# Kernel tuning notes

Hardware: AMD Instinct MI355X
Metric: run time of the kernel (lower is better)

Reference implementation:

```python
import jax, jax.numpy as jnp
import numpy as np

B, S, CIN, WIDTH, COUT = 8, 256, 3, 64, 1
MODES, BW = 32, 3


def _dct_matrix(n):
    # orthonormal DCT-II matrix; inverse = transpose (DCT-III)
    k = np.arange(n)[:, None].astype(np.float64)
    x = np.arange(n)[None, :].astype(np.float64)
    m = np.sqrt(2.0 / n) * np.cos(np.pi * (x + 0.5) * k / n)
    m[0] *= 1.0 / np.sqrt(2.0)
    return jnp.asarray(m, dtype=jnp.float32)

DCT = _dct_matrix(S)  # [S, S]


def T_fwd(u):  # u: [B, C, H, W] -> spectral coefficients
    u = jnp.einsum('kh,bchw->bckw', DCT, u)
    return jnp.einsum('lw,bckw->bckl', DCT, u)


def T_inv(c):  # inverse transform (orthonormal => transpose)
    c = jnp.einsum('kh,bckw->bchw', DCT, c)
    return jnp.einsum('lw,bclw->bclh', DCT, c).transpose(0, 1, 3, 2)


def T_inv2(c):
    # straightforward version: apply M^T along both spatial dims
    c = jnp.einsum('kh,bckl->bchl', DCT, c)
    return jnp.einsum('lw,bchl->bchw', DCT, c)


def gelu(x):
    return jax.nn.gelu(x, approximate=False)


def pseudo_spectra(u, w, cout):
    # u: [B, Cin, S, S]; w: [Cin*BW*BW, cout, MODES*MODES]
    b = T_fwd(u)
    p = MODES + BW - 1
    bp = b[:, :, :p, :p]  # pad_slices (triL=0)
    # im2col matching torch.nn.Unfold channel-major ordering (c, ki, kj)
    patches = jnp.stack([bp[:, :, i:i + MODES, j:j + MODES]
                         for i in range(BW) for j in range(BW)], axis=2)
    bs, cin = u.shape[0], u.shape[1]
    xp = patches.reshape(bs, cin * BW * BW, MODES * MODES)
    om = jnp.einsum('bix,iox->box', xp, w).reshape(bs, cout, MODES, MODES)
    out = jnp.zeros((bs, cout, S, S), u.dtype).at[:, :, :MODES, :MODES].set(om)
    return T_inv2(out)


def conv1x1(x, w, b):
    return jnp.einsum('oi,bihw->bohw', w, x) + b[None, :, None, None]


def setup_inputs() -> dict:
    key = jax.random.key(0)
    ks = jax.random.split(key, 20)
    mm = MODES * MODES
    inp = {'x': jax.random.normal(ks[0], (B, S, S, CIN), dtype=jnp.float32)}
    # PseudoSpectra weights: scale * U[0,1), scale = 1/(in*out)
    inp['wl'] = jax.random.uniform(ks[1], (CIN * BW * BW, WIDTH - CIN, mm), dtype=jnp.float32) / (CIN * (WIDTH - CIN))
    for i in range(4):
        inp[f'wc{i}'] = jax.random.uniform(ks[2 + i], (WIDTH * BW * BW, WIDTH, mm), dtype=jnp.float32) / (WIDTH * WIDTH)
    for i in range(4):
        inp[f'pw{i}'] = jax.random.normal(ks[6 + i], (WIDTH, WIDTH), dtype=jnp.float32) * 0.05
        inp[f'pb{i}'] = jnp.zeros((WIDTH,), dtype=jnp.float32)
    inp['fc1_w'] = jax.random.normal(ks[10], (WIDTH, 128), dtype=jnp.float32) * 0.05
    inp['fc1_b'] = jnp.zeros((128,), dtype=jnp.float32)
    inp['fc2_w'] = jax.random.normal(ks[11], (128, COUT), dtype=jnp.float32) * 0.05
    inp['fc2_b'] = jnp.zeros((COUT,), dtype=jnp.float32)
    return inp


def reference(x, wl, wc0, wc1, wc2, wc3,
              pw0, pb0, pw1, pb1, pw2, pb2, pw3, pb3,
              fc1_w, fc1_b, fc2_w, fc2_b):
    h = x.transpose(0, 3, 1, 2)  # [B, CIN, S, S]
    h = jnp.concatenate([h, gelu(pseudo_spectra(h, wl, WIDTH - CIN))], axis=1)
    h = h + gelu(conv1x1(h, pw0, pb0) + pseudo_spectra(h, wc0, WIDTH))
    h = h + gelu(conv1x1(h, pw1, pb1) + pseudo_spectra(h, wc1, WIDTH))
    h = h + gelu(conv1x1(h, pw2, pb2) + pseudo_spectra(h, wc2, WIDTH))
    h = h + gelu(conv1x1(h, pw3, pb3) + pseudo_spectra(h, wc3, WIDTH))
    h = h.transpose(0, 2, 3, 1)  # [B, S, S, WIDTH]
    h = gelu(h @ fc1_w + fc1_b)
    h = h @ fc2_w + fc2_b  # [B, S, S, COUT]
    y = h.transpose(0, 3, 1, 2)
    y = T_fwd(T_inv2(y))  # T(T.inv(.)) along spatial dims, as in source
    return y.transpose(0, 2, 3, 1)
```

## Files before the change

kernel.cpp:

```cpp
#include <hip/hip_runtime.h>
#include <math.h>

#define BB 8
#define S 256
#define CIN 3
#define W64 64
#define MODES 32
#define PP 34
#define KPAD 36
#define KPB 40

typedef __attribute__((ext_vector_type(8))) short bfrag;
typedef __attribute__((ext_vector_type(16))) float f32x16;

__device__ __forceinline__ float gelu_f(float x){
    float z = fabsf(x) * 0.70710678118654752f;
    float t = 1.0f / (1.0f + 0.3275911f * z);
    float p = ((((1.061405429f * t - 1.453152027f) * t) + 1.421413741f) * t
               - 0.284496736f) * t + 0.254829592f;
    float e = __expf(-z * z);
    float erf = 1.0f - p * t * e;
    erf = copysignf(erf, x);
    return 0.5f * x * (1.0f + erf);
}

__device__ __forceinline__ void split_bf(float x, short &hi, short &lo){
    unsigned u = __float_as_uint(x);
    unsigned r = u + 0x7FFFu + ((u >> 16) & 1u);
    hi = (short)(r >> 16);
    float hf = __uint_as_float(r & 0xFFFF0000u);
    float l = x - hf;
    unsigned v = __float_as_uint(l);
    unsigned s2 = v + 0x7FFFu + ((v >> 16) & 1u);
    lo = (short)(s2 >> 16);
}

__global__ void k_init_dt(float* __restrict__ dt, short* __restrict__ dth,
                          short* __restrict__ dtl){
    int tid = blockIdx.x * 256 + threadIdx.x;
    if (tid >= S * KPB) return;
    int h = tid / KPB, k = tid % KPB;
    double v = 0.0;
    if (k < PP) {
        v = sqrt(2.0 / (double)S) * cos(3.14159265358979323846 * (h + 0.5) * k / (double)S);
        if (k == 0) v *= 0.70710678118654752440;
    }
    float f = (float)v;
    if (k < KPAD) dt[h * KPAD + k] = f;
    short hi, lo; split_bf(f, hi, lo);
    dth[tid] = hi; dtl[tid] = lo;
}

__global__ void k_prep_pw(const float* __restrict__ pw, short* __restrict__ pwh,
                          short* __restrict__ pwl){
    int e = blockIdx.x * 256 + threadIdx.x;
    if (e >= 4096) return;
    short hi, lo; split_bf(pw[e], hi, lo);
    pwh[e] = hi; pwl[e] = lo;
}

__global__ void k_prep_fc1(const float* __restrict__ fc1w, short* __restrict__ f1h,
                           short* __restrict__ f1l){
    int e = blockIdx.x * 256 + threadIdx.x;
    if (e >= 8192) return;
    int i = e >> 7, j = e & 127;
    int n = j >> 5, ks = i >> 4;
    int l = (j & 31) + (((i & 15) >= 8) ? 32 : 0);
    int jr = i & 7;
    int idx = ((n * 4 + ks) * 64 + l) * 8 + jr;
    short hi, lo; split_bf(fc1w[e], hi, lo);
    f1h[idx] = hi; f1l[idx] = lo;
}

__global__ void k_copy_x(const float* __restrict__ x, float* __restrict__ h){
    int e = blockIdx.x * 256 + threadIdx.x;
    if (e >= BB * S * S * CIN) return;
    int px = e / CIN, c = e % CIN;
    h[(size_t)px * W64 + c] = x[e];
}

template<int C>
__global__ void k_fwd1(const float* __restrict__ src, float* __restrict__ tmp1,
                       const float* __restrict__ dt){
    int b = blockIdx.y;
    int idx = blockIdx.x * 256 + threadIdx.x;
    if (idx >= S * C) return;
    float acc[PP];
    #pragma unroll
    for (int k = 0; k < PP; k++) acc[k] = 0.f;
    const float* sp = src + (size_t)b * S * S * C + idx;
    for (int hh = 0; hh < S; hh++){
        float v = sp[(size_t)hh * S * C];
        const float* dr = dt + hh * KPAD;
        #pragma unroll
        for (int k = 0; k < PP; k++) acc[k] = fmaf(dr[k], v, acc[k]);
    }
    float* op = tmp1 + (size_t)b * PP * S * C + idx;
    #pragma unroll
    for (int k = 0; k < PP; k++) op[(size_t)k * S * C] = acc[k];
}

__global__ void k_fwd2_3(const float* __restrict__ tmp1, float* __restrict__ bp,
                         const float* __restrict__ dt){
    const int C = 3;
    int b = blockIdx.y;
    int idx = blockIdx.x * 256 + threadIdx.x;
    if (idx >= PP * C) return;
    int k = idx / C, c = idx % C;
    float acc[PP];
    #pragma unroll
    for (int l = 0; l < PP; l++) acc[l] = 0.f;
    const float* sp = tmp1 + ((size_t)b * PP + k) * S * C + c;
    for (int w = 0; w < S; w++){
        float v = sp[(size_t)w * C];
        const float* dr = dt + w * KPAD;
        #pragma unroll
        for (int l = 0; l < PP; l++) acc[l] = fmaf(dr[l], v, acc[l]);
    }
    float* op = bp + ((size_t)b * PP + k) * PP * C + c;
    #pragma unroll
    for (int l = 0; l < PP; l++) op[(size_t)l * C] = acc[l];
}

__global__ __launch_bounds__(256, 4) void k_fwd2_64(
        const float* __restrict__ tmp1, float* __restrict__ bp,
        const float* __restrict__ dt){
    const int C = 64;
    __shared__ float red[4 * PP * 66];
    int k = blockIdx.x, b = blockIdx.y;
    int t = threadIdx.x;
    int c = t & 63;
    int ws = __builtin_amdgcn_readfirstlane(t >> 6);
    float acc[PP];
    #pragma unroll
    for (int l = 0; l < PP; l++) acc[l] = 0.f;
    const float* sp = tmp1 + ((size_t)b * PP + k) * S * C + c;
    for (int w = ws * 64; w < ws * 64 + 64; w++){
        float v = sp[(size_t)w * C];
        const float* dr = dt + w * KPAD;
        #pragma unroll
        for (int l = 0; l < PP; l++) acc[l] = fmaf(dr[l], v, acc[l]);
    }
    #pragma unroll
    for (int l = 0; l < PP; l++) red[(ws * PP + l) * 66 + c] = acc[l];
    __syncthreads();
    float* op = bp + ((size_t)b * PP + k) * PP * C;
    for (int e = t; e < PP * C; e += 256){
        int l = e >> 6, cc = e & 63;
        op[e] = red[(0 * PP + l) * 66 + cc] + red[(1 * PP + l) * 66 + cc]
              + red[(2 * PP + l) * 66 + cc] + red[(3 * PP + l) * 66 + cc];
    }
}

template<int C, int CC>
__global__ void k_xp_gather(const float* __restrict__ bp, float* __restrict__ xp){
    __shared__ float lds[8 * 3 * PP * (CC + 1)];
    int k  = blockIdx.x;
    int c0 = blockIdx.y * CC;
    int t  = threadIdx.x;
    const int TOT = 8 * 3 * PP * CC;
    for (int e = t; e < TOT; e += 256){
        int b   = e / (3 * PP * CC);
        int r   = e % (3 * PP * CC);
        int row = r / (PP * CC);
        int r2  = r % (PP * CC);
        int l   = r2 / CC;
        int c   = r2 % CC;
        lds[((b * 3 + row) * PP + l) * (CC + 1) + c] =
            bp[(((size_t)b * PP + (k + row)) * PP + l) * C + c0 + c];
    }
    __syncthreads();
    int l = t >> 3;
    int b = t & 7;
    for (int c = 0; c < CC; c++){
        #pragma unroll
        for (int ij = 0; ij < 9; ij++){
            int i_ = ij / 3, j_ = ij % 3;
            int i  = (c0 + c) * 9 + ij;
            float v = lds[((b * 3 + i_) * PP + (l + j_)) * (CC + 1) + c];
            xp[((size_t)i * 1024 + k * 32 + l) * 8 + b] = v;
        }
    }
}

template<int ITOT, int O>
__global__ void k_om(const float* __restrict__ xp, const float* __restrict__ w,
                     float* __restrict__ part){
    int bx  = blockIdx.x;
    int klt = bx & 31;
    int ot  = (bx >> 5) & 7;
    int ns  = bx >> 8;
    const int ILEN = ITOT / 3;
    int t  = threadIdx.x;
    int kl = klt * 32 + (t & 31);
    int o  = ot * 8 + (t >> 5);
    if (o >= O) return;
    float a0=0,a1=0,a2=0,a3=0,a4=0,a5=0,a6=0,a7=0;
    const float* xpp = xp + ((size_t)(ns * ILEN) * 1024 + kl) * 8;
    const float* wp  = w + ((size_t)(ns * ILEN) * O + o) * 1024 + kl;
    #pragma unroll 4
    for (int i = 0; i < ILEN; i++){
        float4 xa = *(const float4*)(xpp + (size_t)i * 8192);
        float4 xb = *(const float4*)(xpp + (size_t)i * 8192 + 4);
        float wv  = wp[(size_t)i * O * 1024];
        a0 = fmaf(xa.x, wv, a0); a1 = fmaf(xa.y, wv, a1);
        a2 = fmaf(xa.z, wv, a2); a3 = fmaf(xa.w, wv, a3);
        a4 = fmaf(xb.x, wv, a4); a5 = fmaf(xb.y, wv, a5);
        a6 = fmaf(xb.z, wv, a6); a7 = fmaf(xb.w, wv, a7);
    }
    float* pp = part + (size_t)ns * 8 * 64 * 1024;
    pp[((size_t)0 * 64 + o) * 1024 + kl] = a0;
    pp[((size_t)1 * 64 + o) * 1024 + kl] = a1;
    pp[((size_t)2 * 64 + o) * 1024 + kl] = a2;
    pp[((size_t)3 * 64 + o) * 1024 + kl] = a3;
    pp[((size_t)4 * 64 + o) * 1024 + kl] = a4;
    pp[((size_t)5 * 64 + o) * 1024 + kl] = a5;
    pp[((size_t)6 * 64 + o) * 1024 + kl] = a6;
    pp[((size_t)7 * 64 + o) * 1024 + kl] = a7;
}

template<int O>
__global__ void k_inv1(const float* __restrict__ part, float* __restrict__ t2,
                       const float* __restrict__ dt){
    __shared__ float oms[32 * 65];
    const int N = 8 * 64 * 1024;
    int wc = blockIdx.x, k = blockIdx.y, b = blockIdx.z;
    int t = threadIdx.x;
    for (int e = t; e < 2048; e += 256){
        int o_ = e >> 5, l = e & 31;
        int idx = ((b * 64 + o_) << 10) + k * 32 + l;
        oms[l * 65 + o_] = part[idx] + part[N + idx] + part[2 * N + idx];
    }
    __syncthreads();
    int o  = t & 63;
    int wg = __builtin_amdgcn_readfirstlane(t >> 6);
    int wbase = wc * 32 + wg * 8;
    float acc[8];
    #pragma unroll
    for (int wj = 0; wj < 8; wj++) acc[wj] = 0.f;
    for (int l = 0; l < 32; l++){
        float ov = oms[l * 65 + o];
        #pragma unroll
        for (int wj = 0; wj < 8; wj++)
            acc[wj] = fmaf(dt[(wbase + wj) * KPAD + l], ov, acc[wj]);
    }
    if (o < O){
        #pragma unroll
        for (int wj = 0; wj < 8; wj++)
            t2[(((size_t)b * 32 + k) * S + wbase + wj) * 64 + o] = acc[wj];
    }
}

template<bool CONV>
__global__ __launch_bounds__(256, 3) void k_fused(
        const float* __restrict__ t2, float* __restrict__ h,
        const short* __restrict__ pwh, const short* __restrict__ pwl,
        const float* __restrict__ pb,
        const short* __restrict__ dth, const short* __restrict__ dtl){
    __shared__ short t2fh[4 * 2 * 64 * 8];
    __shared__ short t2fl[4 * 2 * 64 * 8];
    __shared__ short hsfh[CONV ? 2 * 4 * 64 * 8 : 1];
    __shared__ short hsfl[CONV ? 2 * 4 * 64 * 8 : 1];
    __shared__ float hres[CONV ? 64 * 64 : 1];
    int wt = blockIdx.x, b = blockIdx.y;
    int t = threadIdx.x;

    for (int e = t; e < 1024; e += 256){
        int k = e >> 5, r = e & 31;
        float4 v = *(const float4*)(t2 +
            ((size_t)(b * 32 + k) * S + wt * 2 + (r >> 4)) * 64 + (r & 15) * 4);
        int ks = k >> 4, j = k & 7;
        int lh = ((k & 15) >= 8) ? 32 : 0;
        int wl_ = r >> 4;
        float xs[4] = {v.x, v.y, v.z, v.w};
        #pragma unroll
        for (int q = 0; q < 4; q++){
            int o = (r & 15) * 4 + q;
            int n = (wl_ << 1) | (o >> 5);
            int idx = ((n * 2 + ks) * 64 + (o & 31) + lh) * 8 + j;
            short hi, lo; split_bf(xs[q], hi, lo);
            t2fh[idx] = hi; t2fl[idx] = lo;
        }
    }

    int l = t & 63;
    int n = t >> 6;
    int oh = n & 1, wl = n >> 1;
    int o = oh * 32 + (l & 31);

    for (int ht = 0; ht < 8; ht++){
        if (CONV){
            __syncthreads();
            const float* hbase = h + (((size_t)b * S + ht * 32) * S + wt * 2) * 64;
            for (int e = t; e < 1024; e += 256){
                int px = e >> 4, i4 = e & 15;
                int hh = px >> 1, wl_ = px & 1;
                float4 v = *(const float4*)(hbase + ((size_t)hh * S + wl_) * 64 + i4 * 4);
                *(float4*)(hres + px * 64 + i4 * 4) = v;
                int ks = i4 >> 2;
                int lh = ((i4 & 3) >= 2) ? 32 : 0;
                int jb = (i4 & 1) * 4;
                int base2 = ((wl_ * 4 + ks) * 64 + hh + lh) * 8 + jb;
                short h0,l0,h1,l1,h2,l2,h3,l3;
                split_bf(v.x, h0, l0); split_bf(v.y, h1, l1);
                split_bf(v.z, h2, l2); split_bf(v.w, h3, l3);
                hsfh[base2+0]=h0; hsfh[base2+1]=h1; hsfh[base2+2]=h2; hsfh[base2+3]=h3;
                hsfl[base2+0]=l0; hsfl[base2+1]=l1; hsfl[base2+2]=l2; hsfl[base2+3]=l3;
            }
        }
        __syncthreads();

        f32x16 acc = {0,0,0,0,0,0,0,0,0,0,0,0,0,0,0,0};

        int hh0 = ht * 32;
        #pragma unroll
        for (int ks = 0; ks < 2; ks++){
            int aoff = (hh0 + (l & 31)) * KPB + ks * 16 + (l >> 5) * 8;
            bfrag ah = *(const bfrag*)(dth + aoff);
            bfrag al = *(const bfrag*)(dtl + aoff);
            int boff = ((n * 2 + ks) * 64 + l) * 8;
            bfrag bh = *(const bfrag*)(t2fh + boff);
            bfrag bl = *(const bfrag*)(t2fl + boff);
            acc = __builtin_amdgcn_mfma_f32_32x32x16_bf16(ah, bh, acc, 0, 0, 0);
            acc = __builtin_amdgcn_mfma_f32_32x32x16_bf16(ah, bl, acc, 0, 0, 0);
            acc = __builtin_amdgcn_mfma_f32_32x32x16_bf16(al, bh, acc, 0, 0, 0);
        }

        if (CONV){
            #pragma unroll
            for (int ks = 0; ks < 4; ks++){
                int aoff = ((wl * 4 + ks) * 64 + l) * 8;
                bfrag ah = *(const bfrag*)(hsfh + aoff);
                bfrag al = *(const bfrag*)(hsfl + aoff);
                int boff = (o) * 64 + ks * 16 + (l >> 5) * 8;
                bfrag bh = *(const bfrag*)(pwh + boff);
                bfrag bl = *(const bfrag*)(pwl + boff);
                acc = __builtin_amdgcn_mfma_f32_32x32x16_bf16(ah, bh, acc, 0, 0, 0);
                acc = __builtin_amdgcn_mfma_f32_32x32x16_bf16(ah, bl, acc, 0, 0, 0);
                acc = __builtin_amdgcn_mfma_f32_32x32x16_bf16(al, bh, acc, 0, 0, 0);
            }
            float pbv = pb[o];
            #pragma unroll
            for (int r = 0; r < 16; r++){
                int row = (r & 3) + 8 * (r >> 2) + 4 * (l >> 5);
                float res = hres[(row * 2 + wl) * 64 + o];
                size_t pix = ((size_t)b * S + ht * 32 + row) * S + wt * 2 + wl;
                h[pix * 64 + o] = res + gelu_f(acc[r] + pbv);
            }
        } else {
            if (o < 61){
                #pragma unroll
                for (int r = 0; r < 16; r++){
                    int row = (r & 3) + 8 * (r >> 2) + 4 * (l >> 5);
                    size_t pix = ((size_t)b * S + ht * 32 + row) * S + wt * 2 + wl;
                    h[pix * 64 + 3 + o] = gelu_f(acc[r]);
                }
            }
        }
    }
}

__global__ __launch_bounds__(256, 4) void k_mlp(
        const float* __restrict__ h, const short* __restrict__ f1h,
        const short* __restrict__ f1l, const float* __restrict__ fc1b,
        const float* __restrict__ fc2w, const float* __restrict__ fc2b,
        float* __restrict__ out){
    __shared__ short ah_[2 * 4 * 64 * 8];
    __shared__ short al_[2 * 4 * 64 * 8];
    __shared__ float red[2 * 64 * 33];
    size_t base = (size_t)blockIdx.x * 64;
    int t = threadIdx.x;
    const float* hrow = h + base * 64;
    for (int e = t; e < 1024; e += 256){
        int px = e >> 4, i4 = e & 15;
        float4 v = *(const float4*)(hrow + px * 64 + i4 * 4);
        int ks = i4 >> 2;
        int lh = ((i4 & 3) >= 2) ? 32 : 0;
        int jb = (i4 & 1) * 4;
        int m = px >> 5;
        int idx = ((m * 4 + ks) * 64 + (px & 31) + lh) * 8 + jb;
        short h0,l0,h1,l1,h2,l2,h3,l3;
        split_bf(v.x, h0, l0); split_bf(v.y, h1, l1);
        split_bf(v.z, h2, l2); split_bf(v.w, h3, l3);
        ah_[idx+0]=h0; ah_[idx+1]=h1; ah_[idx+2]=h2; ah_[idx+3]=h3;
        al_[idx+0]=l0; al_[idx+1]=l1; al_[idx+2]=l2; al_[idx+3]=l3;
    }
    __syncthreads();
    int l = t & 63;
    int w = t >> 6;
    int m = w >> 1;
    int n0 = (w & 1) * 2;
    f32x16 acc0 = {0,0,0,0,0,0,0,0,0,0,0,0,0,0,0,0};
    f32x16 acc1 = {0,0,0,0,0,0,0,0,0,0,0,0,0,0,0,0};
    #pragma unroll
    for (int ks = 0; ks < 4; ks++){
        int aoff = ((m * 4 + ks) * 64 + l) * 8;
        bfrag ah = *(const bfrag*)(ah_ + aoff);
        bfrag al = *(const bfrag*)(al_ + aoff);
        int b0off = ((n0 * 4 + ks) * 64 + l) * 8;
        int b1off = (((n0 + 1) * 4 + ks) * 64 + l) * 8;
        bfrag b0h = *(const bfrag*)(f1h + b0off);
        bfrag b0l = *(const bfrag*)(f1l + b0off);
        bfrag b1h = *(const bfrag*)(f1h + b1off);
        bfrag b1l = *(const bfrag*)(f1l + b1off);
        acc0 = __builtin_amdgcn_mfma_f32_32x32x16_bf16(ah, b0h, acc0, 0, 0, 0);
        acc0 = __builtin_amdgcn_mfma_f32_32x32x16_bf16(ah, b0l, acc0, 0, 0, 0);
        acc0 = __builtin_amdgcn_mfma_f32_32x32x16_bf16(al, b0h, acc0, 0, 0, 0);
        acc1 = __builtin_amdgcn_mfma_f32_32x32x16_bf16(ah, b1h, acc1, 0, 0, 0);
        acc1 = __builtin_amdgcn_mfma_f32_32x32x16_bf16(ah, b1l, acc1, 0, 0, 0);
        acc1 = __builtin_amdgcn_mfma_f32_32x32x16_bf16(al, b1h, acc1, 0, 0, 0);
    }
    int j0 = n0 * 32 + (l & 31), j1 = j0 + 32;
    float b10 = fc1b[j0], b11 = fc1b[j1];
    float f20 = fc2w[j0], f21 = fc2w[j1];
    float* rb = red + (w & 1) * 64 * 33;
    #pragma unroll
    for (int r = 0; r < 16; r++){
        int row = (r & 3) + 8 * (r >> 2) + 4 * (l >> 5);
        rb[(m * 32 + row) * 33 + (l & 31)] =
            gelu_f(acc0[r] + b10) * f20 + gelu_f(acc1[r] + b11) * f21;
    }
    __syncthreads();
    if (t < 64){
        float s = fc2b[0];
        #pragma unroll
        for (int c = 0; c < 32; c++)
            s += red[t * 33 + c] + red[(64 + t) * 33 + c];
        out[base + t] = s;
    }
}

extern "C" void kernel_launch(void* const* d_in, const int* in_sizes, int n_in,
                              void* d_out, int out_size, void* d_ws, size_t ws_size,
                              hipStream_t stream) {
    const float* x    = (const float*)d_in[0];
    const float* wl   = (const float*)d_in[1];
    const float* wc[4] = {(const float*)d_in[2], (const float*)d_in[3],
                          (const float*)d_in[4], (const float*)d_in[5]};
    const float* pw[4] = {(const float*)d_in[6], (const float*)d_in[8],
                          (const float*)d_in[10], (const float*)d_in[12]};
    const float* pb[4] = {(const float*)d_in[7], (const float*)d_in[9],
                          (const float*)d_in[11], (const float*)d_in[13]};
    const float* fc1w = (const float*)d_in[14];
    const float* fc1b = (const float*)d_in[15];
    const float* fc2w = (const float*)d_in[16];
    const float* fc2b = (const float*)d_in[17];
    float* out = (float*)d_out;

    char* ws = (char*)d_ws;
    size_t off = 0;
    float* dt   = (float*)(ws + off); off += (size_t)S * KPAD * 4;
    short* dth  = (short*)(ws + off); off += (size_t)S * KPB * 2;
    short* dtl  = (short*)(ws + off); off += (size_t)S * KPB * 2;
    short* pwh  = (short*)(ws + off); off += (size_t)4 * 4096 * 2;
    short* pwl  = (short*)(ws + off); off += (size_t)4 * 4096 * 2;
    short* f1h  = (short*)(ws + off); off += (size_t)8192 * 2;
    short* f1l  = (short*)(ws + off); off += (size_t)8192 * 2;
    float* h    = (float*)(ws + off); off += (size_t)BB * S * S * W64 * 4;
    float* tmp1 = (float*)(ws + off); off += (size_t)BB * PP * S * W64 * 4;
    float* bp   = (float*)(ws + off); off += (size_t)BB * PP * PP * W64 * 4;
    float* xp   = (float*)(ws + off); off += (size_t)576 * 1024 * 8 * 4;
    float* part = (float*)(ws + off); off += (size_t)3 * 8 * 64 * 1024 * 4;
    float* t2   = (float*)(ws + off); off += (size_t)BB * 32 * S * W64 * 4;

    k_init_dt<<<(S * KPB + 255) / 256, 256, 0, stream>>>(dt, dth, dtl);
    for (int i = 0; i < 4; i++)
        k_prep_pw<<<16, 256, 0, stream>>>(pw[i], pwh + i * 4096, pwl + i * 4096);
    k_prep_fc1<<<32, 256, 0, stream>>>(fc1w, f1h, f1l);
    k_copy_x<<<(BB * S * S * CIN + 255) / 256, 256, 0, stream>>>(x, h);

    k_fwd1<3><<<dim3(3, BB), 256, 0, stream>>>(x, tmp1, dt);
    k_fwd2_3<<<dim3(1, BB), 256, 0, stream>>>(tmp1, bp, dt);
    k_xp_gather<3, 3><<<dim3(32, 1), 256, 0, stream>>>(bp, xp);
    k_om<27, 61><<<768, 256, 0, stream>>>(xp, wl, part);
    k_inv1<61><<<dim3(8, 32, BB), 256, 0, stream>>>(part, t2, dt);
    k_fused<false><<<dim3(128, BB), 256, 0, stream>>>(
        t2, h, nullptr, nullptr, nullptr, dth, dtl);

    for (int blk = 0; blk < 4; blk++){
        k_fwd1<64><<<dim3(64, BB), 256, 0, stream>>>(h, tmp1, dt);
        k_fwd2_64<<<dim3(PP, BB), 256, 0, stream>>>(tmp1, bp, dt);
        k_xp_gather<64, 16><<<dim3(32, 4), 256, 0, stream>>>(bp, xp);
        k_om<576, 64><<<768, 256, 0, stream>>>(xp, wc[blk], part);
        k_inv1<64><<<dim3(8, 32, BB), 256, 0, stream>>>(part, t2, dt);
        k_fused<true><<<dim3(128, BB), 256, 0, stream>>>(
            t2, h, pwh + blk * 4096, pwl + blk * 4096, pb[blk], dth, dtl);
    }

    k_mlp<<<dim3(BB * S * S / 64), 256, 0, stream>>>(h, f1h, f1l, fc1b, fc2w, fc2b, out);
}
```

Baseline: 1.327 ms.

## Vectorize LDS fragment stores and prefetch next h tile in fused kernel

```diff
diff --git a/kernel.cpp b/kernel.cpp
--- a/kernel.cpp
+++ b/kernel.cpp
@@ -33,6 +33,18 @@
     unsigned v = __float_as_uint(l);
     unsigned s2 = v + 0x7FFFu + ((v >> 16) & 1u);
     lo = (short)(s2 >> 16);
+}
+
+__device__ __forceinline__ void split8(float4 a, float4 b, bfrag &hv, bfrag &lv){
+    short hi, lo;
+    split_bf(a.x, hi, lo); hv[0] = hi; lv[0] = lo;
+    split_bf(a.y, hi, lo); hv[1] = hi; lv[1] = lo;
+    split_bf(a.z, hi, lo); hv[2] = hi; lv[2] = lo;
+    split_bf(a.w, hi, lo); hv[3] = hi; lv[3] = lo;
+    split_bf(b.x, hi, lo); hv[4] = hi; lv[4] = lo;
+    split_bf(b.y, hi, lo); hv[5] = hi; lv[5] = lo;
+    split_bf(b.z, hi, lo); hv[6] = hi; lv[6] = lo;
+    split_bf(b.w, hi, lo); hv[7] = hi; lv[7] = lo;
 }
 
 __global__ void k_init_dt(float* __restrict__ dt, short* __restrict__ dth,
@@ -257,30 +269,31 @@
         const short* __restrict__ pwh, const short* __restrict__ pwl,
         const float* __restrict__ pb,
         const short* __restrict__ dth, const short* __restrict__ dtl){
-    __shared__ short t2fh[4 * 2 * 64 * 8];
-    __shared__ short t2fl[4 * 2 * 64 * 8];
-    __shared__ short hsfh[CONV ? 2 * 4 * 64 * 8 : 1];
-    __shared__ short hsfl[CONV ? 2 * 4 * 64 * 8 : 1];
+    __shared__ short t2fh[8 * 64 * 8];
+    __shared__ short t2fl[8 * 64 * 8];
+    __shared__ short hsfh[CONV ? 8 * 64 * 8 : 1];
+    __shared__ short hsfl[CONV ? 8 * 64 * 8 : 1];
     __shared__ float hres[CONV ? 64 * 64 : 1];
     int wt = blockIdx.x, b = blockIdx.y;
     int t = threadIdx.x;
 
-    for (int e = t; e < 1024; e += 256){
-        int k = e >> 5, r = e & 31;
-        float4 v = *(const float4*)(t2 +
-            ((size_t)(b * 32 + k) * S + wt * 2 + (r >> 4)) * 64 + (r & 15) * 4);
-        int ks = k >> 4, j = k & 7;
-        int lh = ((k & 15) >= 8) ? 32 : 0;
-        int wl_ = r >> 4;
-        float xs[4] = {v.x, v.y, v.z, v.w};
-        #pragma unroll
-        for (int q = 0; q < 4; q++){
-            int o = (r & 15) * 4 + q;
-            int n = (wl_ << 1) | (o >> 5);
-            int idx = ((n * 2 + ks) * 64 + (o & 31) + lh) * 8 + j;
-            short hi, lo; split_bf(xs[q], hi, lo);
-            t2fh[idx] = hi; t2fl[idx] = lo;
+    #pragma unroll
+    for (int e2 = 0; e2 < 2; e2++){
+        int e = t + e2 * 256;
+        int le = e & 63, ks = (e >> 6) & 1, ne = e >> 7;
+        int oe = (ne & 1) * 32 + (le & 31);
+        int we = wt * 2 + (ne >> 1);
+        int k0 = ks * 16 + (le >> 5) * 8;
+        bfrag hv, lv;
+        #pragma unroll
+        for (int j = 0; j < 8; j++){
+            short hi, lo;
+            split_bf(t2[((size_t)(b * 32 + k0 + j) * S + we) * 64 + oe], hi, lo);
+            hv[j] = hi; lv[j] = lo;
         }
+        int idx = ((ne * 2 + ks) * 64 + le) * 8;
+        *(bfrag*)(t2fh + idx) = hv;
+        *(bfrag*)(t2fl + idx) = lv;
     }
 
     int l = t & 63;
@@ -288,27 +301,46 @@
     int oh = n & 1, wl = n >> 1;
     int o = oh * 32 + (l & 31);
 
+    int ihalf = t & 7;
+    int pxA = t >> 3;
+    int pxB = pxA + 32;
+    const float* hb = h + ((size_t)b * S * S + (size_t)wt * 2) * 64;
+    size_t offA = ((size_t)(pxA >> 1) * S + (pxA & 1)) * 64 + ihalf * 8;
+    size_t offB = ((size_t)(pxB >> 1) * S + (pxB & 1)) * 64 + ihalf * 8;
+    float4 a0, a1, b0, b1;
+    if (CONV){
+        a0 = *(const float4*)(hb + offA);
+        a1 = *(const float4*)(hb + offA + 4);
+        b0 = *(const float4*)(hb + offB);
+        b1 = *(const float4*)(hb + offB + 4);
+    }
+
     for (int ht = 0; ht < 8; ht++){
         if (CONV){
-            __syncthreads();
-            const float* hbase = h + (((size_t)b * S + ht * 32) * S + wt * 2) * 64;
-            for (int e = t; e < 1024; e += 256){
-                int px = e >> 4, i4 = e & 15;
-                int hh = px >> 1, wl_ = px & 1;
-                float4 v = *(const float4*)(hbase + ((size_t)hh * S + wl_) * 64 + i4 * 4);
-                *(float4*)(hres + px * 64 + i4 * 4) = v;
-                int ks = i4 >> 2;
-                int lh = ((i4 & 3) >= 2) ? 32 : 0;
-                int jb = (i4 & 1) * 4;
-                int base2 = ((wl_ * 4 + ks) * 64 + hh + lh) * 8 + jb;
-                short h0,l0,h1,l1,h2,l2,h3,l3;
-                split_bf(v.x, h0, l0); split_bf(v.y, h1, l1);
-                split_bf(v.z, h2, l2); split_bf(v.w, h3, l3);
-                hsfh[base2+0]=h0; hsfh[base2+1]=h1; hsfh[base2+2]=h2; hsfh[base2+3]=h3;
-                hsfl[base2+0]=l0; hsfl[base2+1]=l1; hsfl[base2+2]=l2; hsfl[base2+3]=l3;
-            }
+            int ks = ihalf >> 1;
+            int lh = (ihalf & 1) * 32;
+            bfrag hv, lv;
+            split8(a0, a1, hv, lv);
+            int idx = (((pxA & 1) * 4 + ks) * 64 + (pxA >> 1) + lh) * 8;
+            *(bfrag*)(hsfh + idx) = hv;
+            *(bfrag*)(hsfl + idx) = lv;
+            *(float4*)(hres + pxA * 64 + ihalf * 8)     = a0;
+            *(float4*)(hres + pxA * 64 + ihalf * 8 + 4) = a1;
+            split8(b0, b1, hv, lv);
+            idx = (((pxB & 1) * 4 + ks) * 64 + (pxB >> 1) + lh) * 8;
+            *(bfrag*)(hsfh + idx) = hv;
+            *(bfrag*)(hsfl + idx) = lv;
+            *(float4*)(hres + pxB * 64 + ihalf * 8)     = b0;
+            *(float4*)(hres + pxB * 64 + ihalf * 8 + 4) = b1;
         }
         __syncthreads();
+        if (CONV && ht < 7){
+            const float* hb2 = hb + (size_t)(ht + 1) * 32 * S * 64;
+            a0 = *(const float4*)(hb2 + offA);
+            a1 = *(const float4*)(hb2 + offA + 4);
+            b0 = *(const float4*)(hb2 + offB);
+            b1 = *(const float4*)(hb2 + offB + 4);
+        }
 
         f32x16 acc = {0,0,0,0,0,0,0,0,0,0,0,0,0,0,0,0};
 
@@ -332,7 +364,7 @@
                 int aoff = ((wl * 4 + ks) * 64 + l) * 8;
                 bfrag ah = *(const bfrag*)(hsfh + aoff);
                 bfrag al = *(const bfrag*)(hsfl + aoff);
-                int boff = (o) * 64 + ks * 16 + (l >> 5) * 8;
+                int boff = o * 64 + ks * 16 + (l >> 5) * 8;
                 bfrag bh = *(const bfrag*)(pwh + boff);
                 bfrag bl = *(const bfrag*)(pwl + boff);
                 acc = __builtin_amdgcn_mfma_f32_32x32x16_bf16(ah, bh, acc, 0, 0, 0);
@@ -357,6 +389,7 @@
                 }
             }
         }
+        __syncthreads();
     }
 }
 
@@ -371,19 +404,18 @@
     size_t base = (size_t)blockIdx.x * 64;
     int t = threadIdx.x;
     const float* hrow = h + base * 64;
-    for (int e = t; e < 1024; e += 256){
-        int px = e >> 4, i4 = e & 15;
-        float4 v = *(const float4*)(hrow + px * 64 + i4 * 4);
-        int ks = i4 >> 2;
-        int lh = ((i4 & 3) >= 2) ? 32 : 0;
-        int jb = (i4 & 1) * 4;
-        int m = px >> 5;
-        int idx = ((m * 4 + ks) * 64 + (px & 31) + lh) * 8 + jb;
-        short h0,l0,h1,l1,h2,l2,h3,l3;
-        split_bf(v.x, h0, l0); split_bf(v.y, h1, l1);
-        split_bf(v.z, h2, l2); split_bf(v.w, h3, l3);
-        ah_[idx+0]=h0; ah_[idx+1]=h1; ah_[idx+2]=h2; ah_[idx+3]=h3;
-        al_[idx+0]=l0; al_[idx+1]=l1; al_[idx+2]=l2; al_[idx+3]=l3;
+    #pragma unroll
+    for (int e2 = 0; e2 < 2; e2++){
+        int e = t + e2 * 256;
+        int px = e >> 3, ih = e & 7;
+        float4 v0 = *(const float4*)(hrow + px * 64 + ih * 8);
+        float4 v1 = *(const float4*)(hrow + px * 64 + ih * 8 + 4);
+        bfrag hv, lv;
+        split8(v0, v1, hv, lv);
+        int ks = ih >> 1, lh = (ih & 1) * 32, m = px >> 5;
+        int idx = ((m * 4 + ks) * 64 + (px & 31) + lh) * 8;
+        *(bfrag*)(ah_ + idx) = hv;
+        *(bfrag*)(al_ + idx) = lv;
     }
     __syncthreads();
     int l = t & 63;
```

Measured after the change: 1.268 ms. 4.5% less time.
